# Performance work log

Hardware: AMD Instinct MI355X
Metric: run time of the kernel (lower is better)

Reference implementation:

```python
import jax, jax.numpy as jnp
import numpy as np

# Dimensions (match init_kwargs / input_specs)
B, T, HW, K, J = 8192, 64, 8, 64, 3
FILT_LEN = 8
NEG_SLOPE = 0.001
DWT_OUT_LEN = 84  # lo(14) + hi1(35) + hi2(21) + hi3(14)

# db4 analysis filters (pywt dec_lo / dec_hi)
DB4_LO = np.array([-0.010597401784997278, 0.032883011666982945,
                   0.030841381835986965, -0.18703481171888114,
                   -0.02798376941698385, 0.6308807679295904,
                   0.7148465705525415, 0.23037781330885523], dtype=np.float32)
DB4_HI = np.array([-0.23037781330885523, 0.7148465705525415,
                   -0.6308807679295904, -0.02798376941698385,
                   0.18703481171888114, 0.030841381835986965,
                   0.032883011666982945, -0.010597401784997278], dtype=np.float32)
# pytorch_wavelets stores filters reversed and uses conv1d (cross-correlation)
_H = jnp.asarray(np.ascontiguousarray(np.stack([DB4_LO[::-1], DB4_HI[::-1]])[:, None, :]))  # [2,1,8]


def _afb1d(x):
    # Single-level analysis filter bank along last axis, reflect padding, stride 2.
    # x: [N, n] -> (lo, hi) each [N, floor((n+7)/2)]
    n = x.shape[-1]
    out = (n + FILT_LEN - 1) // 2
    p = 2 * (out - 1) - n + FILT_LEN
    xp = jnp.pad(x, ((0, 0), (p // 2, (p + 1) // 2)), mode='reflect')
    y = jax.lax.conv_general_dilated(xp[:, None, :], _H, (2,), 'VALID')  # [N,2,out]
    return y[:, 0], y[:, 1]


def _dwt(x):
    # J-level DWT; concat [lo_J, hi_1, hi_2, ..., hi_J] along last axis -> [N, 84]
    lo, his = x, []
    for _ in range(J):
        lo, hi = _afb1d(lo)
        his.append(hi)
    return jnp.concatenate([lo] + his, axis=-1)


def setup_inputs() -> dict:
    key = jax.random.key(0)
    k1, k2 = jax.random.split(key)
    x = jax.random.normal(k1, (B, 1, T, HW, HW), dtype=jnp.float32)
    fan_in = DWT_OUT_LEN * HW * HW
    conv_w = jax.random.normal(k2, (K, DWT_OUT_LEN, HW, HW), dtype=jnp.float32) / np.sqrt(fan_in).astype(np.float32)
    conv_b = jnp.zeros((K,), dtype=jnp.float32)
    return {"x": x, "conv_w": conv_w, "conv_b": conv_b}


def reference(x, conv_w, conv_b):
    # x: [B,1,T,H,W]; time_interval=1 and spatial_maxpool_size=1 -> no-ops.
    b = x.shape[0]
    # DWT along time for every (batch, spatial) signal, fully batched.
    sig = x[:, 0].transpose(0, 2, 3, 1).reshape(b * HW * HW, T)  # [B*H*W, T]
    coeffs = _dwt(sig).reshape(b, HW, HW, DWT_OUT_LEN)           # [B,H,W,84]
    # Conv3d with kernel covering the full (84,8,8) volume == one GEMM per output channel.
    feat = jnp.einsum('bhwt,kthw->bk', coeffs, conv_w) + conv_b  # [B,K]
    # Dropout3d in eval mode is identity; LeakyReLU then flatten -> [B, K]
    return jnp.where(feat >= 0, feat, NEG_SLOPE * feat)
```

## Files before the change

### kernel.cpp

```cpp
#include <hip/hip_runtime.h>
#include <hip/hip_bf16.h>

typedef __attribute__((ext_vector_type(4))) float floatx4;
typedef __attribute__((ext_vector_type(8))) short shortx8;

constexpr float CLO[8] = {
    -0.010597401784997278f, 0.032883011666982945f,
     0.030841381835986965f, -0.18703481171888114f,
    -0.02798376941698385f,  0.6308807679295904f,
     0.7148465705525415f,   0.23037781330885523f};
constexpr float CHI[8] = {
    -0.23037781330885523f,  0.7148465705525415f,
    -0.6308807679295904f,  -0.02798376941698385f,
     0.18703481171888114f,  0.030841381835986965f,
     0.032883011666982945f, -0.010597401784997278f};

template <int N, int OUT>
constexpr void afb_c(const float* x, float* lo, float* hi) {
  for (int m = 0; m < OUT; ++m) {
    float aL = 0.f, aH = 0.f;
    for (int i = 0; i < 8; ++i) {
      int s = 2 * m + 1 - i;
      s = (s < 0) ? -s : s;
      s = (s >= N) ? (2 * N - 2 - s) : s;
      aL += CLO[i] * x[s];
      aH += CHI[i] * x[s];
    }
    lo[m] = aL; hi[m] = aH;
  }
}

struct MTab { float v[84][64]; };

constexpr MTab make_M() {
  MTab t{};
  for (int c = 0; c < 64; ++c) {
    float sig[64] = {};
    sig[c] = 1.f;
    float lo1[35] = {}, hi1[35] = {}, lo2[21] = {}, hi2[21] = {};
    float lo3[14] = {}, hi3[14] = {};
    afb_c<64, 35>(sig, lo1, hi1);
    afb_c<35, 21>(lo1, lo2, hi2);
    afb_c<21, 14>(lo2, lo3, hi3);
    for (int m = 0; m < 14; ++m) t.v[m][c]      = lo3[m];
    for (int m = 0; m < 35; ++m) t.v[14 + m][c] = hi1[m];
    for (int m = 0; m < 21; ++m) t.v[49 + m][c] = hi2[m];
    for (int m = 0; m < 14; ++m) t.v[70 + m][c] = hi3[m];
  }
  return t;
}

__device__ __constant__ MTab M_TAB = make_M();

__device__ __forceinline__ unsigned short f2bf_rne(float f) {
  unsigned u = __builtin_bit_cast(unsigned, f);
  unsigned r = (u + 0x7FFFu + ((u >> 16) & 1u)) >> 16;
  return (unsigned short)r;
}

__global__ __launch_bounds__(256) void build_w2_kernel(
    const float* __restrict__ cw, unsigned short* __restrict__ W2) {
  __shared__ float Cl[84 * 64];
  const int k = blockIdx.x;
  const float* cwk = cw + (size_t)k * (84 * 64);
  for (int idx = threadIdx.x; idx < 84 * 64; idx += 256) Cl[idx] = cwk[idx];
  __syncthreads();
  const int tp  = blockIdx.y * 16 + (threadIdx.x >> 4);
  const int hw0 = (threadIdx.x & 15) * 4;
  float a0 = 0.f, a1 = 0.f, a2 = 0.f, a3 = 0.f;
#pragma unroll 4
  for (int t = 0; t < 84; ++t) {
    const float mv = M_TAB.v[t][tp];
    const float4 cv = *(const float4*)&Cl[t * 64 + hw0];
    a0 = fmaf(mv, cv.x, a0);
    a1 = fmaf(mv, cv.y, a1);
    a2 = fmaf(mv, cv.z, a2);
    a3 = fmaf(mv, cv.w, a3);
  }
  uint2 pk;
  pk.x = (unsigned)f2bf_rne(a0) | ((unsigned)f2bf_rne(a1) << 16);
  pk.y = (unsigned)f2bf_rne(a2) | ((unsigned)f2bf_rne(a3) << 16);
  *(uint2*)(W2 + (size_t)k * 4096 + tp * 64 + hw0) = pk;
}

#define KQ_LEN 1024
#define KCHUNK 32

__global__ __launch_bounds__(256, 2) void gemm_kernel(
    const float* __restrict__ A, const unsigned short* __restrict__ W2,
    const float* __restrict__ bias, float* __restrict__ out) {
  __shared__ float part[4 * 64 * 16];

  const int tid  = threadIdx.x;
  const int lane = tid & 63;
  const int kq   = tid >> 6;
  const int frow = lane & 15;
  const int kg   = lane >> 4;

  const float* aptr =
      A + (size_t)(blockIdx.x * 16 + frow) * 4096 + kq * KQ_LEN + kg * 8;
  const unsigned short* bptr =
      W2 + (size_t)frow * 4096 + kq * KQ_LEN + kg * 8;

  floatx4 acc0 = {0.f, 0.f, 0.f, 0.f};
  floatx4 acc1 = {0.f, 0.f, 0.f, 0.f};
  floatx4 acc2 = {0.f, 0.f, 0.f, 0.f};
  floatx4 acc3 = {0.f, 0.f, 0.f, 0.f};

#pragma unroll 2
  for (int i = 0; i < KQ_LEN / KCHUNK; ++i) {
    const int off = i * KCHUNK;
    float4 a0 = *(const float4*)(aptr + off);
    float4 a1 = *(const float4*)(aptr + off + 4);
    uint4 bv0 = *(const uint4*)(bptr + off);
    uint4 bv1 = *(const uint4*)(bptr + 16 * 4096 + off);
    uint4 bv2 = *(const uint4*)(bptr + 32 * 4096 + off);
    uint4 bv3 = *(const uint4*)(bptr + 48 * 4096 + off);
    shortx8 af;
    af[0] = (short)f2bf_rne(a0.x); af[1] = (short)f2bf_rne(a0.y);
    af[2] = (short)f2bf_rne(a0.z); af[3] = (short)f2bf_rne(a0.w);
    af[4] = (short)f2bf_rne(a1.x); af[5] = (short)f2bf_rne(a1.y);
    af[6] = (short)f2bf_rne(a1.z); af[7] = (short)f2bf_rne(a1.w);
    acc0 = __builtin_amdgcn_mfma_f32_16x16x32_bf16(
        af, __builtin_bit_cast(shortx8, bv0), acc0, 0, 0, 0);
    acc1 = __builtin_amdgcn_mfma_f32_16x16x32_bf16(
        af, __builtin_bit_cast(shortx8, bv1), acc1, 0, 0, 0);
    acc2 = __builtin_amdgcn_mfma_f32_16x16x32_bf16(
        af, __builtin_bit_cast(shortx8, bv2), acc2, 0, 0, 0);
    acc3 = __builtin_amdgcn_mfma_f32_16x16x32_bf16(
        af, __builtin_bit_cast(shortx8, bv3), acc3, 0, 0, 0);
  }

  float* pp = &part[(kq * 64 + lane) * 16];
  *(floatx4*)(pp + 0)  = acc0;
  *(floatx4*)(pp + 4)  = acc1;
  *(floatx4*)(pp + 8)  = acc2;
  *(floatx4*)(pp + 12) = acc3;
  __syncthreads();

  const int erow = tid >> 4;
  const int ecg  = (tid & 15) * 4;
  const int nt   = ecg >> 4;
  const int rr   = erow & 3;
  float4 res;
  float* rp = (float*)&res;
#pragma unroll
  for (int j = 0; j < 4; ++j) {
    const int c = ecg + j;
    const int l = ((erow >> 2) << 4) | (c & 15);
    float s = 0.f;
#pragma unroll
    for (int q = 0; q < 4; ++q) s += part[(q * 64 + l) * 16 + nt * 4 + rr];
    const float v = s + bias[c];
    rp[j] = (v >= 0.f) ? v : 0.001f * v;
  }
  *(float4*)(out + (size_t)(blockIdx.x * 16 + erow) * 64 + ecg) = res;
}

extern "C" void kernel_launch(void* const* d_in, const int* in_sizes, int n_in,
                              void* d_out, int out_size, void* d_ws, size_t ws_size,
                              hipStream_t stream) {
  const float* x      = (const float*)d_in[0];
  const float* conv_w = (const float*)d_in[1];
  const float* conv_b = (const float*)d_in[2];
  float* out = (float*)d_out;

  unsigned short* W2 = (unsigned short*)d_ws;

  build_w2_kernel<<<dim3(64, 4), 256, 0, stream>>>(conv_w, W2);
  gemm_kernel<<<512, 256, 0, stream>>>(x, W2, conv_b, out);
}
```

Measured before the change: 220.3 us.

## Stage W2 slice in LDS, split-K across blocks with separate reduce kernel

The GEMM is restructured so each block handles a 64-row tile and one K quarter, staging the 64x1024 bf16 W2 slice in padded shared memory. Eight waves share it, where before every wave streamed W2 directly from global memory. A-operand loads are software-prefetched two iterations ahead. The split-K partials go to a workspace and are summed, with bias and LeakyReLU applied, in a new reduce kernel. This adds an extra launch and 8 MB of partial-sum traffic, and the 132 KB LDS footprint may limit occupancy.

After: 211.2 us. 1.04x faster.

```diff
diff --git a/kernel.cpp b/kernel.cpp
--- a/kernel.cpp
+++ b/kernel.cpp
@@ -83,78 +83,117 @@
   *(uint2*)(W2 + (size_t)k * 4096 + tp * 64 + hw0) = pk;
 }
 
-#define KQ_LEN 1024
-#define KCHUNK 32
-
-__global__ __launch_bounds__(256, 2) void gemm_kernel(
+#define BLDK 1032
+
+__global__ __launch_bounds__(512, 2) void gemm_partial(
     const float* __restrict__ A, const unsigned short* __restrict__ W2,
-    const float* __restrict__ bias, float* __restrict__ out) {
-  __shared__ float part[4 * 64 * 16];
-
-  const int tid  = threadIdx.x;
+    float* __restrict__ pws) {
+  __shared__ alignas(16) char smem[64 * BLDK * 2];
+  short* Bs = (short*)smem;
+  float* part = (float*)smem;
+
+  const int tid = threadIdx.x;
+  const int rowTile = blockIdx.x >> 2;
+  const int kq = blockIdx.x & 3;
+
+#pragma unroll
+  for (int j = 0; j < 16; ++j) {
+    const int idx16 = tid + j * 512;
+    const int n = idx16 >> 7;
+    const int c = (idx16 & 127) * 8;
+    uint4 g = *(const uint4*)(W2 + (size_t)n * 4096 + kq * 1024 + c);
+    *(uint4*)&Bs[n * BLDK + c] = g;
+  }
+  __syncthreads();
+
   const int lane = tid & 63;
-  const int kq   = tid >> 6;
+  const int w = tid >> 6;
+  const int mt = w & 3;
+  const int ks = w >> 2;
   const int frow = lane & 15;
-  const int kg   = lane >> 4;
-
-  const float* aptr =
-      A + (size_t)(blockIdx.x * 16 + frow) * 4096 + kq * KQ_LEN + kg * 8;
-  const unsigned short* bptr =
-      W2 + (size_t)frow * 4096 + kq * KQ_LEN + kg * 8;
+  const int kg = lane >> 4;
+
+  const float* aptr = A + (size_t)(rowTile * 64 + mt * 16 + frow) * 4096 +
+                      kq * 1024 + ks * 512 + kg * 8;
+  const short* bbase = Bs + ks * 512 + kg * 8;
 
   floatx4 acc0 = {0.f, 0.f, 0.f, 0.f};
   floatx4 acc1 = {0.f, 0.f, 0.f, 0.f};
   floatx4 acc2 = {0.f, 0.f, 0.f, 0.f};
   floatx4 acc3 = {0.f, 0.f, 0.f, 0.f};
 
-#pragma unroll 2
-  for (int i = 0; i < KQ_LEN / KCHUNK; ++i) {
-    const int off = i * KCHUNK;
-    float4 a0 = *(const float4*)(aptr + off);
-    float4 a1 = *(const float4*)(aptr + off + 4);
-    uint4 bv0 = *(const uint4*)(bptr + off);
-    uint4 bv1 = *(const uint4*)(bptr + 16 * 4096 + off);
-    uint4 bv2 = *(const uint4*)(bptr + 32 * 4096 + off);
-    uint4 bv3 = *(const uint4*)(bptr + 48 * 4096 + off);
+  float4 a0c = *(const float4*)(aptr);
+  float4 a1c = *(const float4*)(aptr + 4);
+  float4 a0n = *(const float4*)(aptr + 32);
+  float4 a1n = *(const float4*)(aptr + 36);
+
+  for (int i = 0; i < 16; ++i) {
+    const float4 c0 = a0c, c1 = a1c;
+    a0c = a0n; a1c = a1n;
+    if (i + 2 < 16) {
+      a0n = *(const float4*)(aptr + (i + 2) * 32);
+      a1n = *(const float4*)(aptr + (i + 2) * 32 + 4);
+    }
     shortx8 af;
-    af[0] = (short)f2bf_rne(a0.x); af[1] = (short)f2bf_rne(a0.y);
-    af[2] = (short)f2bf_rne(a0.z); af[3] = (short)f2bf_rne(a0.w);
-    af[4] = (short)f2bf_rne(a1.x); af[5] = (short)f2bf_rne(a1.y);
-    af[6] = (short)f2bf_rne(a1.z); af[7] = (short)f2bf_rne(a1.w);
-    acc0 = __builtin_amdgcn_mfma_f32_16x16x32_bf16(
-        af, __builtin_bit_cast(shortx8, bv0), acc0, 0, 0, 0);
-    acc1 = __builtin_amdgcn_mfma_f32_16x16x32_bf16(
-        af, __builtin_bit_cast(shortx8, bv1), acc1, 0, 0, 0);
-    acc2 = __builtin_amdgcn_mfma_f32_16x16x32_bf16(
-        af, __builtin_bit_cast(shortx8, bv2), acc2, 0, 0, 0);
-    acc3 = __builtin_amdgcn_mfma_f32_16x16x32_bf16(
-        af, __builtin_bit_cast(shortx8, bv3), acc3, 0, 0, 0);
-  }
-
-  float* pp = &part[(kq * 64 + lane) * 16];
+    af[0] = (short)f2bf_rne(c0.x); af[1] = (short)f2bf_rne(c0.y);
+    af[2] = (short)f2bf_rne(c0.z); af[3] = (short)f2bf_rne(c0.w);
+    af[4] = (short)f2bf_rne(c1.x); af[5] = (short)f2bf_rne(c1.y);
+    af[6] = (short)f2bf_rne(c1.z); af[7] = (short)f2bf_rne(c1.w);
+    const short* bp = bbase + i * 32;
+    shortx8 bf0 = *(const shortx8*)(bp + (0 * 16 + frow) * BLDK);
+    shortx8 bf1 = *(const shortx8*)(bp + (1 * 16 + frow) * BLDK);
+    shortx8 bf2 = *(const shortx8*)(bp + (2 * 16 + frow) * BLDK);
+    shortx8 bf3 = *(const shortx8*)(bp + (3 * 16 + frow) * BLDK);
+    acc0 = __builtin_amdgcn_mfma_f32_16x16x32_bf16(af, bf0, acc0, 0, 0, 0);
+    acc1 = __builtin_amdgcn_mfma_f32_16x16x32_bf16(af, bf1, acc1, 0, 0, 0);
+    acc2 = __builtin_amdgcn_mfma_f32_16x16x32_bf16(af, bf2, acc2, 0, 0, 0);
+    acc3 = __builtin_amdgcn_mfma_f32_16x16x32_bf16(af, bf3, acc3, 0, 0, 0);
+  }
+
+  __syncthreads();
+  float* pp = part + (w * 64 + lane) * 16;
   *(floatx4*)(pp + 0)  = acc0;
   *(floatx4*)(pp + 4)  = acc1;
   *(floatx4*)(pp + 8)  = acc2;
   *(floatx4*)(pp + 12) = acc3;
   __syncthreads();
 
-  const int erow = tid >> 4;
-  const int ecg  = (tid & 15) * 4;
-  const int nt   = ecg >> 4;
-  const int rr   = erow & 3;
-  float4 res;
-  float* rp = (float*)&res;
+  const int o = tid * 8;
+  const int row = o >> 6;
+  const int cb = o & 63;
+  const int mt2 = row >> 4, rw = row & 15;
+  const int lh = (rw >> 2) << 4, r = rw & 3;
+  float vals[8];
 #pragma unroll
-  for (int j = 0; j < 4; ++j) {
-    const int c = ecg + j;
-    const int l = ((erow >> 2) << 4) | (c & 15);
-    float s = 0.f;
+  for (int jj = 0; jj < 8; ++jj) {
+    const int c = cb + jj;
+    const int l = lh | (c & 15);
+    const int j = ((c >> 4) << 2) | r;
+    vals[jj] = part[(mt2 * 64 + l) * 16 + j] + part[((mt2 + 4) * 64 + l) * 16 + j];
+  }
+  float* dst = pws + (size_t)kq * 524288 + (size_t)(rowTile * 64 + row) * 64 + cb;
+  *(float4*)(dst + 0) = *(float4*)&vals[0];
+  *(float4*)(dst + 4) = *(float4*)&vals[4];
+}
+
+__global__ __launch_bounds__(256) void reduce_kernel(
+    const float* __restrict__ pws, const float* __restrict__ bias,
+    float* __restrict__ out) {
+  const int f = (blockIdx.x * 256 + threadIdx.x) * 4;
+  float4 s = *(const float4*)(pws + f);
 #pragma unroll
-    for (int q = 0; q < 4; ++q) s += part[(q * 64 + l) * 16 + nt * 4 + rr];
-    const float v = s + bias[c];
-    rp[j] = (v >= 0.f) ? v : 0.001f * v;
-  }
-  *(float4*)(out + (size_t)(blockIdx.x * 16 + erow) * 64 + ecg) = res;
+  for (int q = 1; q < 4; ++q) {
+    const float4 p = *(const float4*)(pws + (size_t)q * 524288 + f);
+    s.x += p.x; s.y += p.y; s.z += p.z; s.w += p.w;
+  }
+  const float4 bv = *(const float4*)(bias + (f & 63));
+  float4 r;
+  r.x = s.x + bv.x; r.y = s.y + bv.y; r.z = s.z + bv.z; r.w = s.w + bv.w;
+  r.x = (r.x >= 0.f) ? r.x : 0.001f * r.x;
+  r.y = (r.y >= 0.f) ? r.y : 0.001f * r.y;
+  r.z = (r.z >= 0.f) ? r.z : 0.001f * r.z;
+  r.w = (r.w >= 0.f) ? r.w : 0.001f * r.w;
+  *(float4*)(out + f) = r;
 }
 
 extern "C" void kernel_launch(void* const* d_in, const int* in_sizes, int n_in,
@@ -165,8 +204,10 @@
   const float* conv_b = (const float*)d_in[2];
   float* out = (float*)d_out;
 
-  unsigned short* W2 = (unsigned short*)d_ws;
+  float* pws = (float*)d_ws;
+  unsigned short* W2 = (unsigned short*)((char*)d_ws + (8 << 20));
 
   build_w2_kernel<<<dim3(64, 4), 256, 0, stream>>>(conv_w, W2);
-  gemm_kernel<<<512, 256, 0, stream>>>(x, W2, conv_b, out);
-}
+  gemm_partial<<<512, 512, 0, stream>>>(x, W2, pws);
+  reduce_kernel<<<512, 256, 0, stream>>>(pws, conv_b, out);
+}
```
